# Optimization experiments

Hardware: AMD Instinct MI355X
Metric: run time of the kernel (lower is better)

## Reference

```python
import jax, jax.numpy as jnp
import numpy as np

N, E, K = 10000, 160000, 5
K3 = K ** 3  # 125 spline kernel entries (kernel_size=5, dim=3)
NUM_CLASSES = 6890
# 8 corner combinations of the degree-1 open B-spline in 3 dims
_COMBOS = jnp.asarray(np.array([[i, j, k] for i in (0, 1) for j in (0, 1) for k in (0, 1)], dtype=np.int32))


def spline_basis(pseudo):
    # pseudo: [E,3] in [0,1]; degree-1 open B-spline, kernel_size K per dim
    p = pseudo * (K - 1)
    lo_f = jnp.floor(p)
    frac = p - lo_f                                   # [E,3]
    lo = jnp.clip(lo_f.astype(jnp.int32), 0, K - 1)    # [E,3]
    hi = jnp.minimum(lo + 1, K - 1)
    w = jnp.stack([1.0 - frac, frac], axis=-1)         # [E,3,2]
    idx = jnp.stack([lo, hi], axis=-1)                 # [E,3,2]
    c = _COMBOS                                        # [8,3]
    b = w[:, 0, c[:, 0]] * w[:, 1, c[:, 1]] * w[:, 2, c[:, 2]]          # [E,8]
    flat = idx[:, 0, c[:, 0]] + K * idx[:, 1, c[:, 1]] + K * K * idx[:, 2, c[:, 2]]  # [E,8]
    return b, flat


def spline_conv(x, src, dst, b, flat, W, root, bias):
    # x: [N,in], W: [K3,in,out], root: [in,out], bias: [out]
    xW = jnp.einsum('ni,kio->nko', x, W)               # [N,K3,out]
    gathered = xW[src[:, None], flat]                  # [E,8,out]
    msg = jnp.einsum('es,eso->eo', b, gathered)        # [E,out]
    agg = jax.ops.segment_sum(msg, dst, num_segments=N)
    deg = jax.ops.segment_sum(jnp.ones((msg.shape[0],), msg.dtype), dst, num_segments=N)
    agg = agg / jnp.maximum(deg, 1.0)[:, None]         # mean aggregation
    return agg + x @ root + bias


def setup_inputs() -> dict:
    key = jax.random.key(0)
    ks = jax.random.split(key, 24)
    s = 0.1
    x = jax.random.normal(ks[0], (N, 1), jnp.float32)
    edge_index = jax.random.randint(ks[1], (2, E), 0, N)
    pseudo = jax.random.uniform(ks[2], (E, 3), dtype=jnp.float32)
    W1 = jax.random.normal(ks[3], (K3, 1, 32), jnp.float32) * s
    root1 = jax.random.normal(ks[4], (1, 32), jnp.float32) * s
    b1 = jnp.zeros((32,), jnp.float32)
    W2 = jax.random.normal(ks[5], (K3, 32, 64), jnp.float32) * s
    root2 = jax.random.normal(ks[6], (32, 64), jnp.float32) * s
    b2 = jnp.zeros((64,), jnp.float32)
    Ws = jax.random.normal(ks[7], (4, K3, 64, 64), jnp.float32) * s  # convs 3-6
    roots = jax.random.normal(ks[8], (4, 64, 64), jnp.float32) * s
    bs = jnp.zeros((4, 64), jnp.float32)
    lin1_w = jax.random.normal(ks[9], (64, 256), jnp.float32) * s
    lin1_b = jnp.zeros((256,), jnp.float32)
    lin2_w = jax.random.normal(ks[10], (256, NUM_CLASSES), jnp.float32) * s
    lin2_b = jnp.zeros((NUM_CLASSES,), jnp.float32)
    return {'x': x, 'edge_index': edge_index, 'pseudo': pseudo,
            'W1': W1, 'root1': root1, 'b1': b1,
            'W2': W2, 'root2': root2, 'b2': b2,
            'Ws': Ws, 'roots': roots, 'bs': bs,
            'lin1_w': lin1_w, 'lin1_b': lin1_b, 'lin2_w': lin2_w, 'lin2_b': lin2_b}


def reference(x, edge_index, pseudo, W1, root1, b1, W2, root2, b2, Ws, roots, bs,
              lin1_w, lin1_b, lin2_w, lin2_b):
    src, dst = edge_index[0], edge_index[1]
    b, flat = spline_basis(pseudo)
    h = jax.nn.elu(spline_conv(x, src, dst, b, flat, W1, root1, b1))
    h = jax.nn.elu(spline_conv(h, src, dst, b, flat, W2, root2, b2))
    for l in range(4):  # convs 3-6, fixed layer loop
        h = jax.nn.elu(spline_conv(h, src, dst, b, flat, Ws[l], roots[l], bs[l]))
    h = jax.nn.elu(h @ lin1_w + lin1_b)
    # dropout is identity in eval mode
    logits = h @ lin2_w + lin2_b
    return jax.nn.log_softmax(logits, axis=-1)
```

## Files before the change

### kernel.cpp

```cpp
#include <hip/hip_runtime.h>
#include <hip/hip_bf16.h>
#include <hip/hip_fp16.h>
#include <math.h>

#define Nn 10000
#define Ee 160000
#define NPB 64
#define NBLK 157
#define NKER 125
#define NBUCK (NBLK * NKER)
#define KCHUNK 16
#define KS ((NKER + KCHUNK - 1) / KCHUNK)

#define MPAD 10048
#define NPAD 6912
#define NCLS 6890

typedef float    f32x4 __attribute__((ext_vector_type(4)));
typedef _Float16 f16x8 __attribute__((ext_vector_type(8)));

__global__ __launch_bounds__(256) void basis_kernel(const float* __restrict__ pseudo,
                                                    float* __restrict__ bw,
                                                    int* __restrict__ fl)
{
    int e = blockIdx.x * 256 + threadIdx.x;
    if (e >= Ee) return;
    float p0 = pseudo[e * 3 + 0] * 4.f;
    float p1 = pseudo[e * 3 + 1] * 4.f;
    float p2 = pseudo[e * 3 + 2] * 4.f;
    float f0 = floorf(p0), f1 = floorf(p1), f2 = floorf(p2);
    float fr0 = p0 - f0, fr1 = p1 - f1, fr2 = p2 - f2;
    int lo0 = (int)f0; lo0 = lo0 < 0 ? 0 : (lo0 > 4 ? 4 : lo0);
    int lo1 = (int)f1; lo1 = lo1 < 0 ? 0 : (lo1 > 4 ? 4 : lo1);
    int lo2 = (int)f2; lo2 = lo2 < 0 ? 0 : (lo2 > 4 ? 4 : lo2);
    int hi0 = lo0 + 1 > 4 ? 4 : lo0 + 1;
    int hi1 = lo1 + 1 > 4 ? 4 : lo1 + 1;
    int hi2 = lo2 + 1 > 4 ? 4 : lo2 + 1;
#pragma unroll
    for (int s = 0; s < 8; ++s) {
        int c0 = (s >> 2) & 1, c1 = (s >> 1) & 1, c2 = s & 1;
        float b = (c0 ? fr0 : 1.f - fr0) * (c1 ? fr1 : 1.f - fr1) * (c2 ? fr2 : 1.f - fr2);
        int f = (c0 ? hi0 : lo0) + 5 * (c1 ? hi1 : lo1) + 25 * (c2 ? hi2 : lo2);
        bw[e * 8 + s] = b;
        fl[e * 8 + s] = f;
    }
}

__global__ __launch_bounds__(256) void deg_kernel(const int* __restrict__ dst, int* __restrict__ degi)
{
    int e = blockIdx.x * 256 + threadIdx.x;
    if (e >= Ee) return;
    atomicAdd(&degi[dst[e]], 1);
}

__global__ __launch_bounds__(256) void invdeg_kernel(const int* __restrict__ degi, float* __restrict__ invdeg)
{
    int n = blockIdx.x * 256 + threadIdx.x;
    if (n >= Nn) return;
    int d = degi[n];
    invdeg[n] = 1.f / (float)(d > 0 ? d : 1);
}

__global__ __launch_bounds__(256) void hist_kernel(const int* __restrict__ dst, const int* __restrict__ fl,
                                                   int* __restrict__ hist)
{
    int t = blockIdx.x * 256 + threadIdx.x;
    if (t >= Ee * 8) return;
    int e = t >> 3;
    int key = (dst[e] >> 6) * NKER + fl[t];
    atomicAdd(&hist[key], 1);
}

__global__ __launch_bounds__(1024) void scan_kernel(const int* __restrict__ hist, int* __restrict__ boff)
{
    const int T = 1024;
    const int per = (NBUCK + T - 1) / T;
    int t = threadIdx.x;
    int beg = t * per;
    int end = beg + per; if (end > NBUCK) end = NBUCK;
    int s = 0;
    for (int i = beg; i < end && i < NBUCK; ++i) s += hist[i];
    __shared__ int tmp[1024];
    tmp[t] = s;
    __syncthreads();
    for (int o2 = 1; o2 < 1024; o2 <<= 1) {
        int v = (t >= o2) ? tmp[t - o2] : 0;
        __syncthreads();
        tmp[t] += v;
        __syncthreads();
    }
    int run = tmp[t] - s;
    for (int i = beg; i < end && i < NBUCK; ++i) { boff[i] = run; run += hist[i]; }
    if (t == T - 1) boff[NBUCK] = run;
}

__global__ __launch_bounds__(256) void fill_kernel(const int* __restrict__ srcA, const int* __restrict__ dstA,
                                                   const float* __restrict__ bw, const int* __restrict__ fl,
                                                   int* __restrict__ cursor, uint2* __restrict__ recs)
{
    int t = blockIdx.x * 256 + threadIdx.x;
    if (t >= Ee * 8) return;
    int e = t >> 3;
    int d = dstA[e];
    int key = (d >> 6) * NKER + fl[t];
    int pos = atomicAdd(&cursor[key], 1);
    unsigned meta = (unsigned)srcA[e] | ((unsigned)(d & 63) << 16);
    recs[pos] = make_uint2(meta, __float_as_uint(bw[t]));
}

template <int CIN>
__global__ __launch_bounds__(256) void wb_kernel(const float* __restrict__ W, _Float16* __restrict__ WB)
{
    constexpr int NKC = CIN / 32;
    int t = blockIdx.x * 256 + threadIdx.x;
    int total = NKER * 4 * NKC * 512;
    if (t >= total) return;
    int j = t & 7;
    int lane = (t >> 3) & 63;
    int rem = t >> 9;
    int kc = rem % NKC; rem /= NKC;
    int nt = rem & 3; rem >>= 2;
    int k = rem;
    int ki = kc * 32 + (lane >> 4) * 8 + j;
    int o  = nt * 16 + (lane & 15);
    WB[t] = (_Float16)W[((size_t)k * CIN + ki) * 64 + o];
}

template <int CIN>
__global__ __launch_bounds__(256, 3) void conv_mfma_kernel(const uint2* __restrict__ recs,
                                                           const int* __restrict__ boff,
                                                           const float* __restrict__ xin,
                                                           const _Float16* __restrict__ WB,
                                                           float* __restrict__ agg)
{
    constexpr int NKC = CIN / 32;
    constexpr int RH  = CIN + 8;
    constexpr int STR = 65;
    constexpr int QG  = CIN / 16;

    __shared__ float aggl[NPB * STR];
    __shared__ __align__(16) _Float16 xh[4][16 * RH];
    __shared__ __align__(16) int dlb[4][16];

    const int blk = blockIdx.x;
    for (int idx = threadIdx.x; idx < NPB * STR; idx += 256) aggl[idx] = 0.f;
    __syncthreads();

    const int lane = threadIdx.x & 63;
    const int wid  = threadIdx.x >> 6;
    const int lq   = lane & 15;
    const int quad = lane >> 4;

    int k0 = blockIdx.y * KCHUNK;
    int k1 = k0 + KCHUNK; if (k1 > NKER) k1 = NKER;

    for (int k = k0 + wid; k < k1; k += 4) {
        const int kk = __builtin_amdgcn_readfirstlane(k);
        const int bidx = blk * NKER + kk;
        const int pb = boff[bidx], pe = boff[bidx + 1];
        if (pb >= pe) continue;

        f16x8 bfr[4][NKC];
        {
            const _Float16* __restrict__ wbk = WB + (size_t)kk * (4 * NKC * 512);
#pragma unroll
            for (int nt = 0; nt < 4; ++nt)
#pragma unroll
                for (int kc = 0; kc < NKC; ++kc)
                    bfr[nt][kc] = *(const f16x8*)(wbk + (size_t)((nt * NKC + kc) * 64 + lane) * 8);
        }

        const int nb = (pe - pb + 15) >> 4;

        f32x4 gx[QG];
        float gwt = 0.f;
        int   gdl = 0;

        auto GATHER = [&](int b) {
            int rid = pb + b * 16 + lq;
            bool v = rid < pe;
            uint2 rr = recs[v ? rid : (pe - 1)];
            gwt = v ? __uint_as_float(rr.y) : 0.f;
            int src = (int)(rr.x & 0xFFFFu);
            gdl = (int)(rr.x >> 16);
            const f32x4* __restrict__ xr = (const f32x4*)(xin + (size_t)src * CIN);
#pragma unroll
            for (int q = 0; q < QG; ++q) gx[q] = xr[quad * QG + q];
        };

        auto STAGE = [&]() {
            _Float16* __restrict__ xw = &xh[wid][lq * RH + quad * (4 * QG)];
#pragma unroll
            for (int h8 = 0; h8 < QG / 2; ++h8) {
                f16x8 hv;
#pragma unroll
                for (int j = 0; j < 4; ++j) {
                    hv[j]     = (_Float16)(gx[2 * h8][j]     * gwt);
                    hv[4 + j] = (_Float16)(gx[2 * h8 + 1][j] * gwt);
                }
                *(f16x8*)(xw + h8 * 8) = hv;
            }
            if (quad == 0) dlb[wid][lq] = gdl;
        };

        GATHER(0);
        for (int b = 0; b < nb; ++b) {
            STAGE();
            if (b + 1 < nb) GATHER(b + 1);

            f16x8 af[NKC];
#pragma unroll
            for (int kc = 0; kc < NKC; ++kc)
                af[kc] = *(const f16x8*)&xh[wid][lq * RH + kc * 32 + quad * 8];

            int4 dlv = *(const int4*)&dlb[wid][quad * 4];
            const int dls[4] = {dlv.x, dlv.y, dlv.z, dlv.w};

            f32x4 acc[4];
#pragma unroll
            for (int nt = 0; nt < 4; ++nt) {
                acc[nt] = (f32x4){0.f, 0.f, 0.f, 0.f};
#pragma unroll
                for (int kc = 0; kc < NKC; ++kc)
                    acc[nt] = __builtin_amdgcn_mfma_f32_16x16x32_f16(af[kc], bfr[nt][kc], acc[nt], 0, 0, 0);
            }

#pragma unroll
            for (int nt = 0; nt < 4; ++nt)
#pragma unroll
                for (int r = 0; r < 4; ++r)
                    atomicAdd(&aggl[dls[r] * STR + nt * 16 + lq], acc[nt][r]);
        }
    }
    __syncthreads();
    for (int idx = threadIdx.x; idx < NPB * 64; idx += 256) {
        int n = blk * NPB + (idx >> 6);
        if (n < Nn) atomicAdd(&agg[n * 64 + (idx & 63)], aggl[(idx >> 6) * STR + (idx & 63)]);
    }
}

__global__ __launch_bounds__(256, 3) void conv1_kernel(const uint2* __restrict__ recs,
                                                       const int* __restrict__ boff,
                                                       const float* __restrict__ xin,
                                                       const float* __restrict__ W,
                                                       float* __restrict__ agg)
{
    constexpr int STR = 33;
    __shared__ float aggl[NPB * STR];
    const int blk = blockIdx.x;
    for (int idx = threadIdx.x; idx < NPB * STR; idx += 256) aggl[idx] = 0.f;
    __syncthreads();

    const int lane = threadIdx.x & 63;
    const int wid  = threadIdx.x >> 6;
    int k0 = blockIdx.y * KCHUNK;
    int k1 = k0 + KCHUNK; if (k1 > NKER) k1 = NKER;

    for (int k = k0 + wid; k < k1; k += 4) {
        const int kk = __builtin_amdgcn_readfirstlane(k);
        const int bidx = blk * NKER + kk;
        const int pb = boff[bidx], pe = boff[bidx + 1];
        if (pb >= pe) continue;
        const float* __restrict__ Wk = W + kk * 32;
        float w[32];
#pragma unroll
        for (int o = 0; o < 32; ++o) w[o] = Wk[o];

        for (int p = pb; p < pe; p += 64) {
            int j = p + lane;
            bool v = j < pe;
            uint2 rr = recs[v ? j : (pe - 1)];
            float wt = v ? __uint_as_float(rr.y) : 0.f;
            float xv = xin[rr.x & 0xFFFFu] * wt;
            int dbase = (int)(rr.x >> 16) * STR;
#pragma unroll
            for (int o = 0; o < 32; ++o)
                atomicAdd(&aggl[dbase + o], xv * w[o]);
        }
    }
    __syncthreads();
    for (int idx = threadIdx.x; idx < NPB * 32; idx += 256) {
        int n = blk * NPB + (idx >> 5);
        if (n < Nn) atomicAdd(&agg[n * 32 + (idx & 31)], aggl[(idx >> 5) * STR + (idx & 31)]);
    }
}

template <int CIN, int COUT>
__global__ __launch_bounds__(256) void epilogue_kernel(const float* __restrict__ agg,
                                                       const float* __restrict__ xin,
                                                       const float* __restrict__ root,
                                                       const float* __restrict__ bias,
                                                       const float* __restrict__ invdeg,
                                                       float* __restrict__ out)
{
    int idx = blockIdx.x * 256 + threadIdx.x;
    int n = idx / COUT, o = idx % COUT;
    if (n >= Nn) return;
    float r0 = 0.f, r1 = 0.f;
#pragma unroll
    for (int i = 0; i < CIN; i += 2) {
        r0 += xin[n * CIN + i] * root[i * COUT + o];
        if (CIN > 1) r1 += xin[n * CIN + i + 1] * root[(i + 1) * COUT + o];
    }
    float v = agg[n * COUT + o] * invdeg[n] + r0 + r1 + bias[o];
    out[n * COUT + o] = v > 0.f ? v : expm1f(v);
}

__global__ __launch_bounds__(256) void lin1_kernel(const float* __restrict__ h,
                                                   const float* __restrict__ w1,
                                                   const float* __restrict__ b1,
                                                   _Float16* __restrict__ out)
{
    int n = blockIdx.x;
    __shared__ float hl[64];
    if (threadIdx.x < 64) hl[threadIdx.x] = h[n * 64 + threadIdx.x];
    __syncthreads();
    int j = threadIdx.x;
    float a0 = b1[j], a1 = 0.f, a2 = 0.f, a3 = 0.f;
#pragma unroll
    for (int i = 0; i < 64; i += 4) {
        a0 += hl[i + 0] * w1[(i + 0) * 256 + j];
        a1 += hl[i + 1] * w1[(i + 1) * 256 + j];
        a2 += hl[i + 2] * w1[(i + 2) * 256 + j];
        a3 += hl[i + 3] * w1[(i + 3) * 256 + j];
    }
    float acc = (a0 + a1) + (a2 + a3);
    float v = acc > 0.f ? acc : expm1f(acc);
    out[(size_t)n * 256 + j] = (_Float16)v;
}

__global__ __launch_bounds__(256) void w2t_kernel(const float* __restrict__ w2,
                                                  _Float16* __restrict__ w2t)
{
    __shared__ float t[32][33];
    int n0 = blockIdx.x * 32;
    int k0 = blockIdx.y * 32;
    int tx = threadIdx.x & 31, ty = threadIdx.x >> 5;
#pragma unroll
    for (int q = 0; q < 4; ++q) {
        int k = k0 + ty + 8 * q, n = n0 + tx;
        t[ty + 8 * q][tx] = (n < NCLS) ? w2[(size_t)k * NCLS + n] : 0.f;
    }
    __syncthreads();
#pragma unroll
    for (int q = 0; q < 4; ++q) {
        int n = n0 + ty + 8 * q;
        w2t[(size_t)n * 256 + k0 + tx] = (_Float16)t[tx][ty + 8 * q];
    }
}

__global__ __launch_bounds__(256) void lin2_mfma_kernel(const _Float16* __restrict__ hf,
                                                        const _Float16* __restrict__ w2t,
                                                        const float* __restrict__ b2,
                                                        float* __restrict__ out)
{
    const int tid  = threadIdx.x;
    const int lane = tid & 63, wid = tid >> 6;
    const int wr = wid & 1, wc = wid >> 1;
    const int quad = lane >> 4, lq = lane & 15;

    const int mbase = blockIdx.x * 64 + wr * 32;
    const int nbase = blockIdx.y * 128 + wc * 64;

    f32x4 acc[2][4];
#pragma unroll
    for (int i = 0; i < 2; ++i)
#pragma unroll
        for (int j = 0; j < 4; ++j) acc[i][j] = (f32x4){0.f, 0.f, 0.f, 0.f};

    for (int kc = 0; kc < 256; kc += 32) {
        f16x8 af[2], bfr[4];
#pragma unroll
        for (int mt = 0; mt < 2; ++mt)
            af[mt] = *(const f16x8*)(hf + (size_t)(mbase + mt * 16 + lq) * 256 + kc + quad * 8);
#pragma unroll
        for (int nt = 0; nt < 4; ++nt)
            bfr[nt] = *(const f16x8*)(w2t + (size_t)(nbase + nt * 16 + lq) * 256 + kc + quad * 8);
#pragma unroll
        for (int mt = 0; mt < 2; ++mt)
#pragma unroll
            for (int nt = 0; nt < 4; ++nt)
                acc[mt][nt] = __builtin_amdgcn_mfma_f32_16x16x32_f16(af[mt], bfr[nt], acc[mt][nt], 0, 0, 0);
    }

#pragma unroll
    for (int nt = 0; nt < 4; ++nt) {
        int col = nbase + nt * 16 + lq;
        if (col >= NCLS) continue;
        float bb = b2[col];
#pragma unroll
        for (int mt = 0; mt < 2; ++mt) {
#pragma unroll
            for (int r = 0; r < 4; ++r) {
                int row = mbase + mt * 16 + quad * 4 + r;
                if (row < Nn) out[(size_t)row * NCLS + col] = acc[mt][nt][r] + bb;
            }
        }
    }
}

__global__ __launch_bounds__(1024) void lsm_kernel(float* __restrict__ out)
{
    int row = blockIdx.x;
    float* p = out + (size_t)row * NCLS;
    __shared__ float red[16];
    int tid = threadIdx.x, lane = tid & 63, wid = tid >> 6;

    float m = -3.4e38f;
    for (int jj = tid; jj < NCLS; jj += 1024) m = fmaxf(m, p[jj]);
#pragma unroll
    for (int off = 32; off > 0; off >>= 1) m = fmaxf(m, __shfl_down(m, off));
    if (lane == 0) red[wid] = m;
    __syncthreads();
    if (tid == 0) {
        float mm = red[0];
        for (int w = 1; w < 16; ++w) mm = fmaxf(mm, red[w]);
        red[0] = mm;
    }
    __syncthreads();
    m = red[0];
    __syncthreads();

    float s = 0.f;
    for (int jj = tid; jj < NCLS; jj += 1024) s += expf(p[jj] - m);
#pragma unroll
    for (int off = 32; off > 0; off >>= 1) s += __shfl_down(s, off);
    if (lane == 0) red[wid] = s;
    __syncthreads();
    if (tid == 0) {
        float ss = 0.f;
        for (int w = 1; w < 16; ++w) ss += red[w];
        red[0] += ss;
    }
    __syncthreads();
    float lse = m + logf(red[0]);
    for (int jj = tid; jj < NCLS; jj += 1024) p[jj] -= lse;
}

extern "C" void kernel_launch(void* const* d_in, const int* in_sizes, int n_in,
                              void* d_out, int out_size, void* d_ws, size_t ws_size,
                              hipStream_t stream)
{
    const float* x      = (const float*)d_in[0];
    const int*   ei     = (const int*)d_in[1];
    const float* pseudo = (const float*)d_in[2];
    const float* W1     = (const float*)d_in[3];
    const float* root1  = (const float*)d_in[4];
    const float* b1     = (const float*)d_in[5];
    const float* W2     = (const float*)d_in[6];
    const float* root2  = (const float*)d_in[7];
    const float* b2     = (const float*)d_in[8];
    const float* Ws     = (const float*)d_in[9];
    const float* roots  = (const float*)d_in[10];
    const float* bs     = (const float*)d_in[11];
    const float* l1w    = (const float*)d_in[12];
    const float* l1b    = (const float*)d_in[13];
    const float* l2w    = (const float*)d_in[14];
    const float* l2b    = (const float*)d_in[15];
    float* out = (float*)d_out;

    const int* srcA = ei;
    const int* dstA = ei + Ee;

    char* base = (char*)d_ws;
    size_t off = 0;
    auto carve = [&](size_t bytes) -> void* {
        void* p = base + off;
        off += (bytes + 255) & ~(size_t)255;
        return p;
    };
    float* bw     = (float*)carve((size_t)Ee * 8 * 4);
    int*   fl     = (int*)carve((size_t)Ee * 8 * 4);
    int*   hist   = (int*)carve((size_t)NBUCK * 4);
    int*   boff   = (int*)carve((size_t)(NBUCK + 1) * 4);
    int*   cursor = (int*)carve((size_t)NBUCK * 4);
    uint2* recs   = (uint2*)carve((size_t)Ee * 8 * 8);
    int*   degi   = (int*)carve((size_t)Nn * 4);
    float* invdeg = (float*)carve((size_t)Nn * 4);
    float* agg    = (float*)carve((size_t)Nn * 64 * 4);
    float* hA     = (float*)carve((size_t)Nn * 64 * 4);
    float* hB     = (float*)carve((size_t)Nn * 64 * 4);
    _Float16* hf  = (_Float16*)carve((size_t)MPAD * 256 * 2);
    _Float16* w2t = (_Float16*)carve((size_t)NPAD * 256 * 2);
    _Float16* wb2 = (_Float16*)carve((size_t)NKER * 4 * 1 * 512 * 2);
    _Float16* wbs = (_Float16*)carve((size_t)4 * NKER * 4 * 2 * 512 * 2);
    (void)ws_size; (void)n_in; (void)in_sizes; (void)out_size;

    hipMemsetAsync(hist, 0, (size_t)NBUCK * 4, stream);
    hipMemsetAsync(degi, 0, (size_t)Nn * 4, stream);
    hipMemsetAsync(hf, 0, (size_t)MPAD * 256 * 2, stream);

    basis_kernel<<<(Ee + 255) / 256, 256, 0, stream>>>(pseudo, bw, fl);
    deg_kernel<<<(Ee + 255) / 256, 256, 0, stream>>>(dstA, degi);
    invdeg_kernel<<<(Nn + 255) / 256, 256, 0, stream>>>(degi, invdeg);
    hist_kernel<<<(Ee * 8 + 255) / 256, 256, 0, stream>>>(dstA, fl, hist);
    scan_kernel<<<1, 1024, 0, stream>>>(hist, boff);
    hipMemcpyAsync(cursor, boff, (size_t)NBUCK * 4, hipMemcpyDeviceToDevice, stream);
    fill_kernel<<<(Ee * 8 + 255) / 256, 256, 0, stream>>>(srcA, dstA, bw, fl, cursor, recs);
    w2t_kernel<<<dim3((NPAD + 31) / 32, 8), 256, 0, stream>>>(l2w, w2t);

    wb_kernel<32><<<(NKER * 4 * 1 * 512 + 255) / 256, 256, 0, stream>>>(W2, wb2);
    for (int l = 0; l < 4; ++l)
        wb_kernel<64><<<(NKER * 4 * 2 * 512 + 255) / 256, 256, 0, stream>>>(
            Ws + (size_t)l * NKER * 64 * 64, wbs + (size_t)l * NKER * 4 * 2 * 512);

    const dim3 cgrid(NBLK, KS);

    hipMemsetAsync(agg, 0, (size_t)Nn * 64 * 4, stream);
    conv1_kernel<<<cgrid, 256, 0, stream>>>(recs, boff, x, W1, agg);
    epilogue_kernel<1, 32><<<(Nn * 32 + 255) / 256, 256, 0, stream>>>(agg, x, root1, b1, invdeg, hA);

    hipMemsetAsync(agg, 0, (size_t)Nn * 64 * 4, stream);
    conv_mfma_kernel<32><<<cgrid, 256, 0, stream>>>(recs, boff, hA, wb2, agg);
    epilogue_kernel<32, 64><<<(Nn * 64 + 255) / 256, 256, 0, stream>>>(agg, hA, root2, b2, invdeg, hB);

    float* cin = hB;
    float* cot = hA;
    for (int l = 0; l < 4; ++l) {
        hipMemsetAsync(agg, 0, (size_t)Nn * 64 * 4, stream);
        conv_mfma_kernel<64><<<cgrid, 256, 0, stream>>>(recs, boff, cin,
                                                        wbs + (size_t)l * NKER * 4 * 2 * 512, agg);
        epilogue_kernel<64, 64><<<(Nn * 64 + 255) / 256, 256, 0, stream>>>(
            agg, cin, roots + (size_t)l * 64 * 64, bs + (size_t)l * 64, invdeg, cot);
        float* t = cin; cin = cot; cot = t;
    }

    lin1_kernel<<<Nn, 256, 0, stream>>>(cin, l1w, l1b, hf);
    lin2_mfma_kernel<<<dim3(MPAD / 64, NPAD / 128), 256, 0, stream>>>(hf, w2t, l2b, out);
    lsm_kernel<<<Nn, 1024, 0, stream>>>(out);
}
```

Baseline: 4.133 ms.

## Gather fp16 activations directly into MFMA fragments, scale weights after MFMA

The epilogue now also writes an fp16 copy of each layer's activations, and the spline conv kernel loads these fp16 rows straight into MFMA A-fragments. This replaces the fp32 gather, convert and LDS staging. Edge records are batched into LDS 256 at a time, and the basis weight is applied to the MFMA output before the LDS atomic instead of to the inputs. KCHUNK is halved and the occupancy hint is raised from 3 to 5 waves, which adds grid parallelism and reduces register pressure. In exchange the epilogue writes extra fp16 data, and the gather is no longer software-pipelined.

```diff
diff --git a/kernel.cpp b/kernel.cpp
--- a/kernel.cpp
+++ b/kernel.cpp
@@ -9,7 +9,7 @@
 #define NBLK 157
 #define NKER 125
 #define NBUCK (NBLK * NKER)
-#define KCHUNK 16
+#define KCHUNK 8
 #define KS ((NKER + KCHUNK - 1) / KCHUNK)
 
 #define MPAD 10048
@@ -127,20 +127,17 @@
 }
 
 template <int CIN>
-__global__ __launch_bounds__(256, 3) void conv_mfma_kernel(const uint2* __restrict__ recs,
+__global__ __launch_bounds__(256, 5) void conv_mfma_kernel(const uint2* __restrict__ recs,
                                                            const int* __restrict__ boff,
-                                                           const float* __restrict__ xin,
+                                                           const _Float16* __restrict__ xin,
                                                            const _Float16* __restrict__ WB,
                                                            float* __restrict__ agg)
 {
     constexpr int NKC = CIN / 32;
-    constexpr int RH  = CIN + 8;
     constexpr int STR = 65;
-    constexpr int QG  = CIN / 16;
 
     __shared__ float aggl[NPB * STR];
-    __shared__ __align__(16) _Float16 xh[4][16 * RH];
-    __shared__ __align__(16) int dlb[4][16];
+    __shared__ uint2 rbuf[4][256];
 
     const int blk = blockIdx.x;
     for (int idx = threadIdx.x; idx < NPB * STR; idx += 256) aggl[idx] = 0.f;
@@ -170,66 +167,46 @@
                     bfr[nt][kc] = *(const f16x8*)(wbk + (size_t)((nt * NKC + kc) * 64 + lane) * 8);
         }
 
-        const int nb = (pe - pb + 15) >> 4;
-
-        f32x4 gx[QG];
-        float gwt = 0.f;
-        int   gdl = 0;
-
-        auto GATHER = [&](int b) {
-            int rid = pb + b * 16 + lq;
-            bool v = rid < pe;
-            uint2 rr = recs[v ? rid : (pe - 1)];
-            gwt = v ? __uint_as_float(rr.y) : 0.f;
-            int src = (int)(rr.x & 0xFFFFu);
-            gdl = (int)(rr.x >> 16);
-            const f32x4* __restrict__ xr = (const f32x4*)(xin + (size_t)src * CIN);
-#pragma unroll
-            for (int q = 0; q < QG; ++q) gx[q] = xr[quad * QG + q];
-        };
-
-        auto STAGE = [&]() {
-            _Float16* __restrict__ xw = &xh[wid][lq * RH + quad * (4 * QG)];
-#pragma unroll
-            for (int h8 = 0; h8 < QG / 2; ++h8) {
-                f16x8 hv;
-#pragma unroll
-                for (int j = 0; j < 4; ++j) {
-                    hv[j]     = (_Float16)(gx[2 * h8][j]     * gwt);
-                    hv[4 + j] = (_Float16)(gx[2 * h8 + 1][j] * gwt);
+        for (int ps = pb; ps < pe; ps += 256) {
+            const int cn = (pe - ps < 256) ? (pe - ps) : 256;
+#pragma unroll
+            for (int i = 0; i < 4; ++i) {
+                int idx = i * 64 + lane;
+                int rid = ps + idx;
+                rbuf[wid][idx] = recs[rid < pe ? rid : pe - 1];
+            }
+            const int nb = (cn + 15) >> 4;
+            for (int b = 0; b < nb; ++b) {
+                const int rbase = b * 16;
+                uint2 rme = rbuf[wid][rbase + lq];
+                int src = (int)(rme.x & 0xFFFFu);
+                f16x8 a[NKC];
+#pragma unroll
+                for (int kc = 0; kc < NKC; ++kc)
+                    a[kc] = *(const f16x8*)(xin + (size_t)src * CIN + kc * 32 + quad * 8);
+
+                uint2 rw[4];
+#pragma unroll
+                for (int r = 0; r < 4; ++r) rw[r] = rbuf[wid][rbase + quad * 4 + r];
+
+                f32x4 acc[4];
+#pragma unroll
+                for (int nt = 0; nt < 4; ++nt) {
+                    acc[nt] = (f32x4){0.f, 0.f, 0.f, 0.f};
+#pragma unroll
+                    for (int kc = 0; kc < NKC; ++kc)
+                        acc[nt] = __builtin_amdgcn_mfma_f32_16x16x32_f16(a[kc], bfr[nt][kc], acc[nt], 0, 0, 0);
                 }
-                *(f16x8*)(xw + h8 * 8) = hv;
+
+#pragma unroll
+                for (int r = 0; r < 4; ++r) {
+                    float wt = (rbase + quad * 4 + r < cn) ? __uint_as_float(rw[r].y) : 0.f;
+                    int db = (int)(rw[r].x >> 16) * STR;
+#pragma unroll
+                    for (int nt = 0; nt < 4; ++nt)
+                        atomicAdd(&aggl[db + nt * 16 + lq], wt * acc[nt][r]);
+                }
             }
-            if (quad == 0) dlb[wid][lq] = gdl;
-        };
-
-        GATHER(0);
-        for (int b = 0; b < nb; ++b) {
-            STAGE();
-            if (b + 1 < nb) GATHER(b + 1);
-
-            f16x8 af[NKC];
-#pragma unroll
-            for (int kc = 0; kc < NKC; ++kc)
-                af[kc] = *(const f16x8*)&xh[wid][lq * RH + kc * 32 + quad * 8];
-
-            int4 dlv = *(const int4*)&dlb[wid][quad * 4];
-            const int dls[4] = {dlv.x, dlv.y, dlv.z, dlv.w};
-
-            f32x4 acc[4];
-#pragma unroll
-            for (int nt = 0; nt < 4; ++nt) {
-                acc[nt] = (f32x4){0.f, 0.f, 0.f, 0.f};
-#pragma unroll
-                for (int kc = 0; kc < NKC; ++kc)
-                    acc[nt] = __builtin_amdgcn_mfma_f32_16x16x32_f16(af[kc], bfr[nt][kc], acc[nt], 0, 0, 0);
-            }
-
-#pragma unroll
-            for (int nt = 0; nt < 4; ++nt)
-#pragma unroll
-                for (int r = 0; r < 4; ++r)
-                    atomicAdd(&aggl[dls[r] * STR + nt * 16 + lq], acc[nt][r]);
         }
     }
     __syncthreads();
@@ -291,7 +268,8 @@
                                                        const float* __restrict__ root,
                                                        const float* __restrict__ bias,
                                                        const float* __restrict__ invdeg,
-                                                       float* __restrict__ out)
+                                                       float* __restrict__ out32,
+                                                       _Float16* __restrict__ out16)
 {
     int idx = blockIdx.x * 256 + threadIdx.x;
     int n = idx / COUT, o = idx % COUT;
@@ -303,7 +281,9 @@
         if (CIN > 1) r1 += xin[n * CIN + i + 1] * root[(i + 1) * COUT + o];
     }
     float v = agg[n * COUT + o] * invdeg[n] + r0 + r1 + bias[o];
-    out[n * COUT + o] = v > 0.f ? v : expm1f(v);
+    v = v > 0.f ? v : expm1f(v);
+    out32[n * COUT + o] = v;
+    out16[n * COUT + o] = (_Float16)v;
 }
 
 __global__ __launch_bounds__(256) void lin1_kernel(const float* __restrict__ h,
@@ -480,6 +460,8 @@
     float* agg    = (float*)carve((size_t)Nn * 64 * 4);
     float* hA     = (float*)carve((size_t)Nn * 64 * 4);
     float* hB     = (float*)carve((size_t)Nn * 64 * 4);
+    _Float16* hA16 = (_Float16*)carve((size_t)Nn * 64 * 2);
+    _Float16* hB16 = (_Float16*)carve((size_t)Nn * 64 * 2);
     _Float16* hf  = (_Float16*)carve((size_t)MPAD * 256 * 2);
     _Float16* w2t = (_Float16*)carve((size_t)NPAD * 256 * 2);
     _Float16* wb2 = (_Float16*)carve((size_t)NKER * 4 * 1 * 512 * 2);
@@ -508,21 +490,22 @@
 
     hipMemsetAsync(agg, 0, (size_t)Nn * 64 * 4, stream);
     conv1_kernel<<<cgrid, 256, 0, stream>>>(recs, boff, x, W1, agg);
-    epilogue_kernel<1, 32><<<(Nn * 32 + 255) / 256, 256, 0, stream>>>(agg, x, root1, b1, invdeg, hA);
+    epilogue_kernel<1, 32><<<(Nn * 32 + 255) / 256, 256, 0, stream>>>(agg, x, root1, b1, invdeg, hA, hA16);
 
     hipMemsetAsync(agg, 0, (size_t)Nn * 64 * 4, stream);
-    conv_mfma_kernel<32><<<cgrid, 256, 0, stream>>>(recs, boff, hA, wb2, agg);
-    epilogue_kernel<32, 64><<<(Nn * 64 + 255) / 256, 256, 0, stream>>>(agg, hA, root2, b2, invdeg, hB);
-
-    float* cin = hB;
-    float* cot = hA;
+    conv_mfma_kernel<32><<<cgrid, 256, 0, stream>>>(recs, boff, hA16, wb2, agg);
+    epilogue_kernel<32, 64><<<(Nn * 64 + 255) / 256, 256, 0, stream>>>(agg, hA, root2, b2, invdeg, hB, hB16);
+
+    float* cin = hB;       float* cot = hA;
+    _Float16* cin16 = hB16; _Float16* cot16 = hA16;
     for (int l = 0; l < 4; ++l) {
         hipMemsetAsync(agg, 0, (size_t)Nn * 64 * 4, stream);
-        conv_mfma_kernel<64><<<cgrid, 256, 0, stream>>>(recs, boff, cin,
+        conv_mfma_kernel<64><<<cgrid, 256, 0, stream>>>(recs, boff, cin16,
                                                         wbs + (size_t)l * NKER * 4 * 2 * 512, agg);
         epilogue_kernel<64, 64><<<(Nn * 64 + 255) / 256, 256, 0, stream>>>(
-            agg, cin, roots + (size_t)l * 64 * 64, bs + (size_t)l * 64, invdeg, cot);
+            agg, cin, roots + (size_t)l * 64 * 64, bs + (size_t)l * 64, invdeg, cot, cot16);
         float* t = cin; cin = cot; cot = t;
+        _Float16* t16 = cin16; cin16 = cot16; cot16 = t16;
     }
 
     lin1_kernel<<<Nn, 256, 0, stream>>>(cin, l1w, l1b, hf);
```

Result: faster. 3.971 ms (-3.9%).
